# Performance work log

Hardware: AMD Instinct MI355X
Metric: run time of the kernel (lower is better)

Reference implementation:

```python
import jax, jax.numpy as jnp
import numpy as np

B = 1024
D = 768          # 2 * hidden_size
HID = 384        # hidden_size (split point for mu/sigma)
MLP_H = 300      # InfoNCE hidden size
LOG2PI = float(np.log(2.0 * np.pi))


def setup_inputs() -> dict:
    key = jax.random.key(0)
    ks = jax.random.split(key, 12)
    s = 0.02
    return {
        "zl": jax.random.normal(ks[0], (B, 20, D), jnp.float32),
        "zv": jax.random.normal(ks[1], (B, 36, D), jnp.float32),
        "fc_l_w": jax.random.normal(ks[2], (20,), jnp.float32) * s,
        "fc_l_b": jax.random.normal(ks[3], (), jnp.float32) * s,
        "fc_v_w": jax.random.normal(ks[4], (36,), jnp.float32) * s,
        "fc_v_b": jax.random.normal(ks[5], (), jnp.float32) * s,
        "W1": jax.random.normal(ks[6], (MLP_H, 2 * HID), jnp.float32) * s,
        "b1": jnp.zeros((MLP_H,), jnp.float32),
        "W2": jax.random.normal(ks[7], (1, MLP_H), jnp.float32) * s,
        "b2": jnp.zeros((1,), jnp.float32),
        "eps1": jax.random.normal(ks[8], (B, HID), jnp.float32),
        "eps2": jax.random.normal(ks[9], (B, HID), jnp.float32),
        "perm": jax.random.permutation(ks[10], B),
    }


def _log_prob(mu, sigma, x):
    # Independent(Normal(mu, sigma), 1).log_prob(x)
    z = (x - mu) / sigma
    return jnp.sum(-jnp.log(sigma) - 0.5 * LOG2PI - 0.5 * z * z, axis=-1)


def reference(zl, zv, fc_l_w, fc_l_b, fc_v_w, fc_v_b, W1, b1, W2, b2, eps1, eps2, perm):
    # fc over token dim: permute(0,2,1) @ Linear(20->1) -> [B, D]
    z1 = jnp.einsum('bsd,s->bd', zl, fc_l_w) + fc_l_b
    z2 = jnp.einsum('bsd,s->bd', zv, fc_v_w) + fc_v_b

    mu1, sig1 = z1[:, :HID], jax.nn.softplus(z1[:, HID:]) + 1e-7
    mu2, sig2 = z2[:, :HID], jax.nn.softplus(z2[:, HID:]) + 1e-7

    # rsample
    s1 = mu1 + sig1 * eps1  # [B, HID]
    s2 = mu2 + sig2 * eps2

    kl_1_2 = _log_prob(mu1, sig1, s1) - _log_prob(mu2, sig2, s1)
    kl_2_1 = _log_prob(mu2, sig2, s2) - _log_prob(mu1, sig1, s2)
    d_skl = jnp.mean(kl_1_2 + kl_2_1) / 2.0

    # InfoNCE(x=s1, y=s2): F(x,y) = softplus(relu([x,y]W1^T + b1) W2^T + b2)
    W1x, W1y = W1[:, :HID], W1[:, HID:]
    Ax = s1 @ W1x.T            # [B, MLP_H], x contribution
    By = s2 @ W1y.T            # [B, MLP_H], y contribution
    w2 = W2[0]                 # [MLP_H]

    # T0: matched pairs
    T0 = jax.nn.softplus(jax.nn.relu(Ax + By + b1) @ w2 + b2[0])  # [B]

    # T1[i, j] = F(x_j, y_perm[i]); tile via broadcasting instead of repeat+cat
    By_p = By[perm]                                             # [B, MLP_H]
    h = jax.nn.relu(Ax[None, :, :] + By_p[:, None, :] + b1)     # [B, B, MLP_H]
    T1 = jax.nn.softplus(h @ w2 + b2[0])                        # [B, B]

    lower_bound = T0.mean() - (jax.scipy.special.logsumexp(T1, axis=1).mean() - jnp.log(jnp.float32(B)))
    return d_skl - lower_bound
```

## Files before the change

kernel.cpp:

```cpp
#include <hip/hip_runtime.h>
#include <math.h>

#define BB   1024
#define DD   768
#define HIDV 384
#define MLPH 300
#define MLPP 320

typedef float v2f __attribute__((ext_vector_type(2)));

typedef const __attribute__((address_space(1))) void* gas_t;
typedef __attribute__((address_space(3))) void* las_t;

__device__ __forceinline__ float softplusf(float x) {
    return (x > 20.f) ? x : log1pf(expf(x));
}

__device__ __forceinline__ void f4arr(float4 v, float* o) {
    o[0] = v.x; o[1] = v.y; o[2] = v.z; o[3] = v.w;
}

__device__ __forceinline__ void cp16(const float* g, float* l) {
    __builtin_amdgcn_global_load_lds((gas_t)g, (las_t)l, 16, 0, 0);
}

#define WAITVM(n)  asm volatile("s_waitcnt vmcnt(" #n ")" ::: "memory")
#define WAITLGKM() asm volatile("s_waitcnt lgkmcnt(0)" ::: "memory")

__global__ void k_init(float* __restrict__ ws) {
    int i = blockIdx.x * 256 + threadIdx.x;
    if (i < 16 + BB) ws[i] = 0.f;
}

__global__ __launch_bounds__(256) void k_rs(
    const float* __restrict__ zl, const float* __restrict__ zv,
    const float* __restrict__ wl, const float* __restrict__ blp,
    const float* __restrict__ wv, const float* __restrict__ bvp,
    const float* __restrict__ eps1, const float* __restrict__ eps2,
    float* __restrict__ s1, float* __restrict__ s2, float* __restrict__ accum)
{
    __shared__ float LA[9216];
    __shared__ float LB[6144];
    int tid = threadIdx.x, w = tid >> 6, l = tid & 63, b = blockIdx.x;

    const float* zlb = zl + b * 15360;
    const float* zvb = zv + b * 27648;
    const float* gA0 = zlb + (w * 5 + 0) * 768 + l * 4;
    const float* gB0 = zlb + (w * 5 + 3) * 768 + l * 4;
    const float* gA1 = zvb + (w * 9 + 0) * 768 + l * 4;
    const float* gB1 = zvb + (w * 9 + 3) * 768 + l * 4;
    const float* gA2 = zvb + (w * 9 + 5) * 768 + l * 4;
    const float* gB2 = zvb + (w * 9 + 8) * 768 + l * 4;
    float* sA = LA + w * 2304;
    float* sB = LB + w * 1536;

    float wl_r[5], wv_r[9];
    #pragma unroll
    for (int r = 0; r < 5; ++r) wl_r[r] = wl[w * 5 + r];
    #pragma unroll
    for (int r = 0; r < 9; ++r) wv_r[r] = wv[w * 9 + r];
    WAITVM(0);

    float a1[3][4] = {{0.f}}, a2[3][4] = {{0.f}};

    #pragma unroll
    for (int r = 0; r < 3; ++r)
        #pragma unroll
        for (int c = 0; c < 3; ++c)
            cp16(gA0 + r * 768 + c * 256, sA + r * 768 + c * 256);
    #pragma unroll
    for (int r = 0; r < 2; ++r)
        #pragma unroll
        for (int c = 0; c < 3; ++c)
            cp16(gB0 + r * 768 + c * 256, sB + r * 768 + c * 256);

    WAITVM(6);
    #pragma unroll
    for (int r = 0; r < 3; ++r) {
        float ws_ = wl_r[r];
        #pragma unroll
        for (int c = 0; c < 3; ++c) {
            float v[4]; f4arr(*(const float4*)(sA + r * 768 + c * 256 + l * 4), v);
            #pragma unroll
            for (int j = 0; j < 4; ++j) a1[c][j] = fmaf(v[j], ws_, a1[c][j]);
        }
    }
    WAITLGKM();
    #pragma unroll
    for (int r = 0; r < 3; ++r)
        #pragma unroll
        for (int c = 0; c < 3; ++c)
            cp16(gA1 + r * 768 + c * 256, sA + r * 768 + c * 256);

    WAITVM(9);
    #pragma unroll
    for (int r = 0; r < 2; ++r) {
        float ws_ = wl_r[3 + r];
        #pragma unroll
        for (int c = 0; c < 3; ++c) {
            float v[4]; f4arr(*(const float4*)(sB + r * 768 + c * 256 + l * 4), v);
            #pragma unroll
            for (int j = 0; j < 4; ++j) a1[c][j] = fmaf(v[j], ws_, a1[c][j]);
        }
    }
    WAITLGKM();
    #pragma unroll
    for (int r = 0; r < 2; ++r)
        #pragma unroll
        for (int c = 0; c < 3; ++c)
            cp16(gB1 + r * 768 + c * 256, sB + r * 768 + c * 256);

    WAITVM(6);
    #pragma unroll
    for (int r = 0; r < 3; ++r) {
        float ws_ = wv_r[r];
        #pragma unroll
        for (int c = 0; c < 3; ++c) {
            float v[4]; f4arr(*(const float4*)(sA + r * 768 + c * 256 + l * 4), v);
            #pragma unroll
            for (int j = 0; j < 4; ++j) a2[c][j] = fmaf(v[j], ws_, a2[c][j]);
        }
    }
    WAITLGKM();
    #pragma unroll
    for (int r = 0; r < 3; ++r)
        #pragma unroll
        for (int c = 0; c < 3; ++c)
            cp16(gA2 + r * 768 + c * 256, sA + r * 768 + c * 256);

    WAITVM(9);
    #pragma unroll
    for (int r = 0; r < 2; ++r) {
        float ws_ = wv_r[3 + r];
        #pragma unroll
        for (int c = 0; c < 3; ++c) {
            float v[4]; f4arr(*(const float4*)(sB + r * 768 + c * 256 + l * 4), v);
            #pragma unroll
            for (int j = 0; j < 4; ++j) a2[c][j] = fmaf(v[j], ws_, a2[c][j]);
        }
    }
    WAITLGKM();
    #pragma unroll
    for (int c = 0; c < 3; ++c)
        cp16(gB2 + c * 256, sB + c * 256);

    WAITVM(3);
    #pragma unroll
    for (int r = 0; r < 3; ++r) {
        float ws_ = wv_r[5 + r];
        #pragma unroll
        for (int c = 0; c < 3; ++c) {
            float v[4]; f4arr(*(const float4*)(sA + r * 768 + c * 256 + l * 4), v);
            #pragma unroll
            for (int j = 0; j < 4; ++j) a2[c][j] = fmaf(v[j], ws_, a2[c][j]);
        }
    }
    WAITVM(0);
    {
        float ws_ = wv_r[8];
        #pragma unroll
        for (int c = 0; c < 3; ++c) {
            float v[4]; f4arr(*(const float4*)(sB + c * 256 + l * 4), v);
            #pragma unroll
            for (int j = 0; j < 4; ++j) a2[c][j] = fmaf(v[j], ws_, a2[c][j]);
        }
    }

    #pragma unroll
    for (int c = 0; c < 3; ++c) {
        *(float4*)(LA + w * 2304 + (c * 64 + l) * 4) =
            make_float4(a1[c][0], a1[c][1], a1[c][2], a1[c][3]);
        *(float4*)(LA + w * 2304 + 768 + (c * 64 + l) * 4) =
            make_float4(a2[c][0], a2[c][1], a2[c][2], a2[c][3]);
    }
    __syncthreads();

    float bl = blp[0], bv = bvp[0];
    float z1v[4] = {0,0,0,0}, z2v[4] = {0,0,0,0};
    if (tid < 192) {
        #pragma unroll
        for (int w2 = 0; w2 < 4; ++w2) {
            float q1[4], q2[4];
            f4arr(*(const float4*)(LA + w2 * 2304 + tid * 4), q1);
            f4arr(*(const float4*)(LA + w2 * 2304 + 768 + tid * 4), q2);
            #pragma unroll
            for (int j = 0; j < 4; ++j) { z1v[j] += q1[j]; z2v[j] += q2[j]; }
        }
    }
    __syncthreads();
    if (tid >= 96 && tid < 192) {
        float o1[4], o2[4];
        #pragma unroll
        for (int j = 0; j < 4; ++j) {
            o1[j] = softplusf(z1v[j] + bl) + 1e-7f;
            o2[j] = softplusf(z2v[j] + bv) + 1e-7f;
        }
        *(float4*)(LB + (tid - 96) * 4)       = make_float4(o1[0], o1[1], o1[2], o1[3]);
        *(float4*)(LB + 384 + (tid - 96) * 4) = make_float4(o2[0], o2[1], o2[2], o2[3]);
    }
    __syncthreads();

    float con = 0.f;
    if (tid < 96) {
        float e1v[4], e2v[4], g1[4], g2[4];
        f4arr(((const float4*)eps1)[b * 96 + tid], e1v);
        f4arr(((const float4*)eps2)[b * 96 + tid], e2v);
        f4arr(*(const float4*)(LB + tid * 4), g1);
        f4arr(*(const float4*)(LB + 384 + tid * 4), g2);
        float s1o[4], s2o[4];
        #pragma unroll
        for (int j = 0; j < 4; ++j) {
            float mu1 = z1v[j] + bl;
            float mu2 = z2v[j] + bv;
            float sg1 = g1[j], sg2 = g2[j];
            float e1 = e1v[j], e2 = e2v[j];
            float sv1 = fmaf(sg1, e1, mu1);
            float sv2 = fmaf(sg2, e2, mu2);
            s1o[j] = sv1; s2o[j] = sv2;
            float z12 = (sv1 - mu2) / sg2;
            float z21 = (sv2 - mu1) / sg1;
            con += -0.5f * (e1 * e1 + e2 * e2) + 0.5f * z12 * z12 + 0.5f * z21 * z21;
        }
        ((float4*)s1)[b * 96 + tid] = make_float4(s1o[0], s1o[1], s1o[2], s1o[3]);
        ((float4*)s2)[b * 96 + tid] = make_float4(s2o[0], s2o[1], s2o[2], s2o[3]);
    }

    #pragma unroll
    for (int m = 1; m < 64; m <<= 1) con += __shfl_xor(con, m);
    __shared__ float pr[4];
    if ((tid & 63) == 0) pr[tid >> 6] = con;
    __syncthreads();
    if (tid == 0) atomicAdd(&accum[0], pr[0] + pr[1] + pr[2] + pr[3]);
}

__global__ __launch_bounds__(256) void k_gemm(
    const float* __restrict__ s1, const float* __restrict__ s2,
    const float* __restrict__ W1, const float* __restrict__ b1,
    float* __restrict__ Axb, float* __restrict__ By)
{
    __shared__ __align__(16) float Ss[32][36];
    __shared__ __align__(16) float Ws[32][68];
    int z = blockIdx.z;
    const float* S = z ? s2 : s1;
    float* Out = z ? By : Axb;
    int wofs = z ? HIDV : 0;
    int b0 = blockIdx.x * 32;
    int k0 = blockIdx.y * 64;
    int tid = threadIdx.x;
    int srow = tid >> 3, sc = tid & 7;
    int wrow = tid >> 2, wc = tid & 3;
    int krow = k0 + wrow;
    int tx = tid & 15, ty = tid >> 4;

    float4 ps, pw[2];
    auto ld = [&](int hc) {
        ps = *(const float4*)&S[(b0 + srow) * HIDV + hc + sc * 4];
        #pragma unroll
        for (int u = 0; u < 2; ++u)
            pw[u] = (krow < MLPH) ? *(const float4*)&W1[krow * DD + wofs + hc + wc * 4 + u * 16]
                                  : make_float4(0.f, 0.f, 0.f, 0.f);
    };
    ld(0);
    v2f acc[2][2];
    acc[0][0] = (v2f){0.f, 0.f}; acc[0][1] = (v2f){0.f, 0.f};
    acc[1][0] = (v2f){0.f, 0.f}; acc[1][1] = (v2f){0.f, 0.f};

    for (int ch = 0; ch < 12; ++ch) {
        __syncthreads();
        Ss[sc * 4 + 0][srow] = ps.x; Ss[sc * 4 + 1][srow] = ps.y;
        Ss[sc * 4 + 2][srow] = ps.z; Ss[sc * 4 + 3][srow] = ps.w;
        #pragma unroll
        for (int u = 0; u < 2; ++u) {
            int hb = wc * 4 + u * 16;
            Ws[hb + 0][wrow] = pw[u].x; Ws[hb + 1][wrow] = pw[u].y;
            Ws[hb + 2][wrow] = pw[u].z; Ws[hb + 3][wrow] = pw[u].w;
        }
        __syncthreads();
        if (ch < 11) ld((ch + 1) * 32);
        #pragma unroll
        for (int h = 0; h < 32; ++h) {
            v2f sv = *(const v2f*)&Ss[h][ty * 2];
            float4 wq = *(const float4*)&Ws[h][tx * 4];
            v2f w0 = (v2f){wq.x, wq.y};
            v2f w1 = (v2f){wq.z, wq.w};
            v2f s0 = (v2f){sv.x, sv.x};
            v2f s1b = (v2f){sv.y, sv.y};
            acc[0][0] = __builtin_elementwise_fma(s0, w0, acc[0][0]);
            acc[0][1] = __builtin_elementwise_fma(s0, w1, acc[0][1]);
            acc[1][0] = __builtin_elementwise_fma(s1b, w0, acc[1][0]);
            acc[1][1] = __builtin_elementwise_fma(s1b, w1, acc[1][1]);
        }
    }
    #pragma unroll
    for (int i = 0; i < 2; ++i) {
        int bb = b0 + ty * 2 + i;
        float vraw[4] = {acc[i][0].x, acc[i][0].y, acc[i][1].x, acc[i][1].y};
        float o[4];
        #pragma unroll
        for (int j = 0; j < 4; ++j) {
            int k = k0 + tx * 4 + j;
            float v = vraw[j];
            if (!z) v += b1[k < MLPH ? k : 0];
            o[j] = (k < MLPH) ? v : 0.f;
        }
        *(float4*)&Out[bb * MLPP + k0 + tx * 4] = make_float4(o[0], o[1], o[2], o[3]);
    }
}

__global__ void k_t0(const float* __restrict__ Axb, const float* __restrict__ By,
                     const float* __restrict__ W2, const float* __restrict__ b2,
                     float* __restrict__ accum)
{
    int b = blockIdx.x;
    int l = threadIdx.x;
    float t = 0.f;
    for (int k = l; k < MLPH; k += 64)
        t = fmaf(fmaxf(Axb[b * MLPP + k] + By[b * MLPP + k], 0.f), W2[k], t);
    #pragma unroll
    for (int m = 1; m < 64; m <<= 1) t += __shfl_xor(t, m);
    if (l == 0) atomicAdd(&accum[1], softplusf(t + b2[0]));
}

__global__ __launch_bounds__(256) void k_pairs(
    const float* __restrict__ Axb, const float* __restrict__ By,
    const int* __restrict__ perm, const float* __restrict__ W2,
    const float* __restrict__ b2, float* __restrict__ sumexp)
{
    __shared__ __align__(16) float As[64][68];
    __shared__ __align__(16) float Bs[64][68];
    __shared__ float w2s[MLPP];
    int tid = threadIdx.x;
    int j0 = blockIdx.x * 64;
    int i0 = blockIdx.y * 64;
    for (int t = tid; t < MLPP; t += 256) w2s[t] = (t < MLPH) ? W2[t] : 0.f;
    int r = tid >> 2;
    int c4 = tid & 3;
    int tx = tid & 15, ty = tid >> 4;
    int prow = perm[i0 + r];

    float4 pa[4], pb[4];
    auto ld = [&](int kc) {
        #pragma unroll
        for (int u = 0; u < 4; ++u) {
            int kq = (c4 + 4 * u) * 4;
            pa[u] = *(const float4*)&Axb[(j0 + r) * MLPP + kc + kq];
            pb[u] = *(const float4*)&By[prow * MLPP + kc + kq];
        }
    };
    ld(0);
    v2f acc2[4][2];
    #pragma unroll
    for (int c = 0; c < 4; ++c) {
        acc2[c][0] = (v2f){0.f, 0.f};
        acc2[c][1] = (v2f){0.f, 0.f};
    }
    for (int ch = 0; ch < 5; ++ch) {
        __syncthreads();
        #pragma unroll
        for (int u = 0; u < 4; ++u) {
            int kq = (c4 + 4 * u) * 4;
            As[kq + 0][r] = pa[u].x; As[kq + 1][r] = pa[u].y;
            As[kq + 2][r] = pa[u].z; As[kq + 3][r] = pa[u].w;
            Bs[kq + 0][r] = pb[u].x; Bs[kq + 1][r] = pb[u].y;
            Bs[kq + 2][r] = pb[u].z; Bs[kq + 3][r] = pb[u].w;
        }
        __syncthreads();
        if (ch < 4) ld((ch + 1) * 64);
        int kc = ch * 64;
        #pragma unroll
        for (int k = 0; k < 64; ++k) {
            float w = w2s[kc + k];
            v2f wv2 = (v2f){w, w};
            float4 af = *(const float4*)&As[k][tx * 4];
            float4 bf = *(const float4*)&Bs[k][ty * 4];
            v2f a2[2] = { (v2f){af.x, af.y}, (v2f){af.z, af.w} };
            float bs[4] = {bf.x, bf.y, bf.z, bf.w};
            #pragma unroll
            for (int c = 0; c < 4; ++c) {
                v2f bc = (v2f){bs[c], bs[c]};
                #pragma unroll
                for (int d2 = 0; d2 < 2; ++d2) {
                    v2f tv = a2[d2] + bc;
                    tv = __builtin_elementwise_max(tv, (v2f){0.f, 0.f});
                    acc2[c][d2] = __builtin_elementwise_fma(tv, wv2, acc2[c][d2]);
                }
            }
        }
    }
    float b2v = b2[0];
    #pragma unroll
    for (int c = 0; c < 4; ++c) {
        float vv[4] = {acc2[c][0].x, acc2[c][0].y, acc2[c][1].x, acc2[c][1].y};
        float ssum = 0.f;
        #pragma unroll
        for (int d = 0; d < 4; ++d)
            ssum += 1.f + expf(vv[d] + b2v);
        ssum += __shfl_xor(ssum, 1);
        ssum += __shfl_xor(ssum, 2);
        ssum += __shfl_xor(ssum, 4);
        ssum += __shfl_xor(ssum, 8);
        if (tx == 0) atomicAdd(&sumexp[i0 + ty * 4 + c], ssum);
    }
}

__global__ __launch_bounds__(256) void k_final(
    const float* __restrict__ accum, const float* __restrict__ sumexp,
    float* __restrict__ out)
{
    int tid = threadIdx.x;
    float s = 0.f;
    for (int i = tid; i < BB; i += 256) s += logf(sumexp[i]);
    #pragma unroll
    for (int m = 1; m < 64; m <<= 1) s += __shfl_xor(s, m);
    __shared__ float red[4];
    if ((tid & 63) == 0) red[tid >> 6] = s;
    __syncthreads();
    if (tid == 0) {
        float lse_mean = (red[0] + red[1] + red[2] + red[3]) / (float)BB;
        float d_skl = accum[0] / (2.f * (float)BB);
        float t0_mean = accum[1] / (float)BB;
        float lower = t0_mean - (lse_mean - logf((float)BB));
        out[0] = d_skl - lower;
    }
}

extern "C" void kernel_launch(void* const* d_in, const int* in_sizes, int n_in,
                              void* d_out, int out_size, void* d_ws, size_t ws_size,
                              hipStream_t stream)
{
    const float* zl     = (const float*)d_in[0];
    const float* zv     = (const float*)d_in[1];
    const float* fc_l_w = (const float*)d_in[2];
    const float* fc_l_b = (const float*)d_in[3];
    const float* fc_v_w = (const float*)d_in[4];
    const float* fc_v_b = (const float*)d_in[5];
    const float* W1     = (const float*)d_in[6];
    const float* b1     = (const float*)d_in[7];
    const float* W2     = (const float*)d_in[8];
    const float* b2     = (const float*)d_in[9];
    const float* eps1   = (const float*)d_in[10];
    const float* eps2   = (const float*)d_in[11];
    const int*   perm   = (const int*)d_in[12];
    float* out = (float*)d_out;

    float* ws     = (float*)d_ws;
    float* accum  = ws;
    float* sumexp = ws + 16;
    float* s1     = ws + 16 + BB;
    float* s2     = s1 + BB * HIDV;
    float* Axb    = s2 + BB * HIDV;
    float* By     = Axb + BB * MLPP;

    k_init<<<5, 256, 0, stream>>>(ws);
    k_rs<<<BB, 256, 0, stream>>>(zl, zv, fc_l_w, fc_l_b, fc_v_w, fc_v_b,
                                 eps1, eps2, s1, s2, accum);
    k_gemm<<<dim3(32, 5, 2), 256, 0, stream>>>(s1, s2, W1, b1, Axb, By);
    k_t0<<<BB, 64, 0, stream>>>(Axb, By, W2, b2, accum);
    k_pairs<<<dim3(16, 16), 256, 0, stream>>>(Axb, By, perm, W2, b2, sumexp);
    k_final<<<1, 256, 0, stream>>>(accum, sumexp, out);
}
```

Measured before the change: 310.7 us.

## Replace LDS-staged token reduction with direct register float4 loads

```diff
diff --git a/kernel.cpp b/kernel.cpp
--- a/kernel.cpp
+++ b/kernel.cpp
@@ -9,211 +9,83 @@
 
 typedef float v2f __attribute__((ext_vector_type(2)));
 
-typedef const __attribute__((address_space(1))) void* gas_t;
-typedef __attribute__((address_space(3))) void* las_t;
-
 __device__ __forceinline__ float softplusf(float x) {
     return (x > 20.f) ? x : log1pf(expf(x));
 }
-
-__device__ __forceinline__ void f4arr(float4 v, float* o) {
-    o[0] = v.x; o[1] = v.y; o[2] = v.z; o[3] = v.w;
-}
-
-__device__ __forceinline__ void cp16(const float* g, float* l) {
-    __builtin_amdgcn_global_load_lds((gas_t)g, (las_t)l, 16, 0, 0);
-}
-
-#define WAITVM(n)  asm volatile("s_waitcnt vmcnt(" #n ")" ::: "memory")
-#define WAITLGKM() asm volatile("s_waitcnt lgkmcnt(0)" ::: "memory")
 
 __global__ void k_init(float* __restrict__ ws) {
     int i = blockIdx.x * 256 + threadIdx.x;
     if (i < 16 + BB) ws[i] = 0.f;
 }
 
-__global__ __launch_bounds__(256) void k_rs(
+__global__ __launch_bounds__(192, 3) void k_rs(
     const float* __restrict__ zl, const float* __restrict__ zv,
     const float* __restrict__ wl, const float* __restrict__ blp,
     const float* __restrict__ wv, const float* __restrict__ bvp,
     const float* __restrict__ eps1, const float* __restrict__ eps2,
     float* __restrict__ s1, float* __restrict__ s2, float* __restrict__ accum)
 {
-    __shared__ float LA[9216];
-    __shared__ float LB[6144];
-    int tid = threadIdx.x, w = tid >> 6, l = tid & 63, b = blockIdx.x;
-
-    const float* zlb = zl + b * 15360;
-    const float* zvb = zv + b * 27648;
-    const float* gA0 = zlb + (w * 5 + 0) * 768 + l * 4;
-    const float* gB0 = zlb + (w * 5 + 3) * 768 + l * 4;
-    const float* gA1 = zvb + (w * 9 + 0) * 768 + l * 4;
-    const float* gB1 = zvb + (w * 9 + 3) * 768 + l * 4;
-    const float* gA2 = zvb + (w * 9 + 5) * 768 + l * 4;
-    const float* gB2 = zvb + (w * 9 + 8) * 768 + l * 4;
-    float* sA = LA + w * 2304;
-    float* sB = LB + w * 1536;
-
-    float wl_r[5], wv_r[9];
-    #pragma unroll
-    for (int r = 0; r < 5; ++r) wl_r[r] = wl[w * 5 + r];
-    #pragma unroll
-    for (int r = 0; r < 9; ++r) wv_r[r] = wv[w * 9 + r];
-    WAITVM(0);
-
-    float a1[3][4] = {{0.f}}, a2[3][4] = {{0.f}};
-
-    #pragma unroll
-    for (int r = 0; r < 3; ++r)
-        #pragma unroll
-        for (int c = 0; c < 3; ++c)
-            cp16(gA0 + r * 768 + c * 256, sA + r * 768 + c * 256);
-    #pragma unroll
-    for (int r = 0; r < 2; ++r)
-        #pragma unroll
-        for (int c = 0; c < 3; ++c)
-            cp16(gB0 + r * 768 + c * 256, sB + r * 768 + c * 256);
-
-    WAITVM(6);
-    #pragma unroll
-    for (int r = 0; r < 3; ++r) {
-        float ws_ = wl_r[r];
-        #pragma unroll
-        for (int c = 0; c < 3; ++c) {
-            float v[4]; f4arr(*(const float4*)(sA + r * 768 + c * 256 + l * 4), v);
-            #pragma unroll
-            for (int j = 0; j < 4; ++j) a1[c][j] = fmaf(v[j], ws_, a1[c][j]);
-        }
-    }
-    WAITLGKM();
-    #pragma unroll
-    for (int r = 0; r < 3; ++r)
-        #pragma unroll
-        for (int c = 0; c < 3; ++c)
-            cp16(gA1 + r * 768 + c * 256, sA + r * 768 + c * 256);
-
-    WAITVM(9);
-    #pragma unroll
-    for (int r = 0; r < 2; ++r) {
-        float ws_ = wl_r[3 + r];
-        #pragma unroll
-        for (int c = 0; c < 3; ++c) {
-            float v[4]; f4arr(*(const float4*)(sB + r * 768 + c * 256 + l * 4), v);
-            #pragma unroll
-            for (int j = 0; j < 4; ++j) a1[c][j] = fmaf(v[j], ws_, a1[c][j]);
-        }
-    }
-    WAITLGKM();
-    #pragma unroll
-    for (int r = 0; r < 2; ++r)
-        #pragma unroll
-        for (int c = 0; c < 3; ++c)
-            cp16(gB1 + r * 768 + c * 256, sB + r * 768 + c * 256);
-
-    WAITVM(6);
-    #pragma unroll
-    for (int r = 0; r < 3; ++r) {
-        float ws_ = wv_r[r];
-        #pragma unroll
-        for (int c = 0; c < 3; ++c) {
-            float v[4]; f4arr(*(const float4*)(sA + r * 768 + c * 256 + l * 4), v);
-            #pragma unroll
-            for (int j = 0; j < 4; ++j) a2[c][j] = fmaf(v[j], ws_, a2[c][j]);
-        }
-    }
-    WAITLGKM();
-    #pragma unroll
-    for (int r = 0; r < 3; ++r)
-        #pragma unroll
-        for (int c = 0; c < 3; ++c)
-            cp16(gA2 + r * 768 + c * 256, sA + r * 768 + c * 256);
-
-    WAITVM(9);
-    #pragma unroll
-    for (int r = 0; r < 2; ++r) {
-        float ws_ = wv_r[3 + r];
-        #pragma unroll
-        for (int c = 0; c < 3; ++c) {
-            float v[4]; f4arr(*(const float4*)(sB + r * 768 + c * 256 + l * 4), v);
-            #pragma unroll
-            for (int j = 0; j < 4; ++j) a2[c][j] = fmaf(v[j], ws_, a2[c][j]);
-        }
-    }
-    WAITLGKM();
-    #pragma unroll
-    for (int c = 0; c < 3; ++c)
-        cp16(gB2 + c * 256, sB + c * 256);
-
-    WAITVM(3);
-    #pragma unroll
-    for (int r = 0; r < 3; ++r) {
-        float ws_ = wv_r[5 + r];
-        #pragma unroll
-        for (int c = 0; c < 3; ++c) {
-            float v[4]; f4arr(*(const float4*)(sA + r * 768 + c * 256 + l * 4), v);
-            #pragma unroll
-            for (int j = 0; j < 4; ++j) a2[c][j] = fmaf(v[j], ws_, a2[c][j]);
-        }
-    }
-    WAITVM(0);
-    {
-        float ws_ = wv_r[8];
-        #pragma unroll
-        for (int c = 0; c < 3; ++c) {
-            float v[4]; f4arr(*(const float4*)(sB + c * 256 + l * 4), v);
-            #pragma unroll
-            for (int j = 0; j < 4; ++j) a2[c][j] = fmaf(v[j], ws_, a2[c][j]);
-        }
-    }
-
-    #pragma unroll
-    for (int c = 0; c < 3; ++c) {
-        *(float4*)(LA + w * 2304 + (c * 64 + l) * 4) =
-            make_float4(a1[c][0], a1[c][1], a1[c][2], a1[c][3]);
-        *(float4*)(LA + w * 2304 + 768 + (c * 64 + l) * 4) =
-            make_float4(a2[c][0], a2[c][1], a2[c][2], a2[c][3]);
-    }
-    __syncthreads();
+    __shared__ float SG[768];
+    __shared__ float pr[3];
+    int tid = threadIdx.x;
+    int b = blockIdx.x;
+
+    const float4* zl4 = (const float4*)(zl + (size_t)b * 15360) + tid;
+    const float4* zv4 = (const float4*)(zv + (size_t)b * 27648) + tid;
+
+    float a1[4] = {0.f, 0.f, 0.f, 0.f};
+    float a2[4] = {0.f, 0.f, 0.f, 0.f};
+
+    #pragma unroll
+    for (int s = 0; s < 20; ++s) {
+        float4 v = zl4[s * 192];
+        float w = wl[s];
+        a1[0] = fmaf(v.x, w, a1[0]);
+        a1[1] = fmaf(v.y, w, a1[1]);
+        a1[2] = fmaf(v.z, w, a1[2]);
+        a1[3] = fmaf(v.w, w, a1[3]);
+    }
+    #pragma unroll
+    for (int s = 0; s < 36; ++s) {
+        float4 v = zv4[s * 192];
+        float w = wv[s];
+        a2[0] = fmaf(v.x, w, a2[0]);
+        a2[1] = fmaf(v.y, w, a2[1]);
+        a2[2] = fmaf(v.z, w, a2[2]);
+        a2[3] = fmaf(v.w, w, a2[3]);
+    }
 
     float bl = blp[0], bv = bvp[0];
-    float z1v[4] = {0,0,0,0}, z2v[4] = {0,0,0,0};
-    if (tid < 192) {
-        #pragma unroll
-        for (int w2 = 0; w2 < 4; ++w2) {
-            float q1[4], q2[4];
-            f4arr(*(const float4*)(LA + w2 * 2304 + tid * 4), q1);
-            f4arr(*(const float4*)(LA + w2 * 2304 + 768 + tid * 4), q2);
-            #pragma unroll
-            for (int j = 0; j < 4; ++j) { z1v[j] += q1[j]; z2v[j] += q2[j]; }
-        }
-    }
-    __syncthreads();
-    if (tid >= 96 && tid < 192) {
+
+    if (tid >= 96) {
         float o1[4], o2[4];
         #pragma unroll
         for (int j = 0; j < 4; ++j) {
-            o1[j] = softplusf(z1v[j] + bl) + 1e-7f;
-            o2[j] = softplusf(z2v[j] + bv) + 1e-7f;
-        }
-        *(float4*)(LB + (tid - 96) * 4)       = make_float4(o1[0], o1[1], o1[2], o1[3]);
-        *(float4*)(LB + 384 + (tid - 96) * 4) = make_float4(o2[0], o2[1], o2[2], o2[3]);
+            o1[j] = softplusf(a1[j] + bl) + 1e-7f;
+            o2[j] = softplusf(a2[j] + bv) + 1e-7f;
+        }
+        *(float4*)(SG + (tid - 96) * 4)       = make_float4(o1[0], o1[1], o1[2], o1[3]);
+        *(float4*)(SG + 384 + (tid - 96) * 4) = make_float4(o2[0], o2[1], o2[2], o2[3]);
     }
     __syncthreads();
 
     float con = 0.f;
     if (tid < 96) {
-        float e1v[4], e2v[4], g1[4], g2[4];
-        f4arr(((const float4*)eps1)[b * 96 + tid], e1v);
-        f4arr(((const float4*)eps2)[b * 96 + tid], e2v);
-        f4arr(*(const float4*)(LB + tid * 4), g1);
-        f4arr(*(const float4*)(LB + 384 + tid * 4), g2);
+        float4 e1v = ((const float4*)eps1)[b * 96 + tid];
+        float4 e2v = ((const float4*)eps2)[b * 96 + tid];
+        float e1a[4] = {e1v.x, e1v.y, e1v.z, e1v.w};
+        float e2a[4] = {e2v.x, e2v.y, e2v.z, e2v.w};
+        float4 g1 = *(const float4*)(SG + tid * 4);
+        float4 g2 = *(const float4*)(SG + 384 + tid * 4);
+        float g1a[4] = {g1.x, g1.y, g1.z, g1.w};
+        float g2a[4] = {g2.x, g2.y, g2.z, g2.w};
         float s1o[4], s2o[4];
         #pragma unroll
         for (int j = 0; j < 4; ++j) {
-            float mu1 = z1v[j] + bl;
-            float mu2 = z2v[j] + bv;
-            float sg1 = g1[j], sg2 = g2[j];
-            float e1 = e1v[j], e2 = e2v[j];
+            float mu1 = a1[j] + bl;
+            float mu2 = a2[j] + bv;
+            float sg1 = g1a[j], sg2 = g2a[j];
+            float e1 = e1a[j], e2 = e2a[j];
             float sv1 = fmaf(sg1, e1, mu1);
             float sv2 = fmaf(sg2, e2, mu2);
             s1o[j] = sv1; s2o[j] = sv2;
@@ -227,10 +99,9 @@
 
     #pragma unroll
     for (int m = 1; m < 64; m <<= 1) con += __shfl_xor(con, m);
-    __shared__ float pr[4];
     if ((tid & 63) == 0) pr[tid >> 6] = con;
     __syncthreads();
-    if (tid == 0) atomicAdd(&accum[0], pr[0] + pr[1] + pr[2] + pr[3]);
+    if (tid == 0) atomicAdd(&accum[0], pr[0] + pr[1] + pr[2]);
 }
 
 __global__ __launch_bounds__(256) void k_gemm(
@@ -452,7 +323,7 @@
     float* By     = Axb + BB * MLPP;
 
     k_init<<<5, 256, 0, stream>>>(ws);
-    k_rs<<<BB, 256, 0, stream>>>(zl, zv, fc_l_w, fc_l_b, fc_v_w, fc_v_b,
+    k_rs<<<BB, 192, 0, stream>>>(zl, zv, fc_l_w, fc_l_b, fc_v_w, fc_v_b,
                                  eps1, eps2, s1, s2, accum);
     k_gemm<<<dim3(32, 5, 2), 256, 0, stream>>>(s1, s2, W1, b1, Axb, By);
     k_t0<<<BB, 64, 0, stream>>>(Axb, By, W2, b2, accum);
```

Result: no change. 310.6 us (-0.0%).
